# Kernel tuning notes

Measured on AMD Instinct MI355X. Metric: run time of the kernel, lower is better.

## Reference

```python
import jax, jax.numpy as jnp
import numpy as np
import math

EMBED_DIM = 2048
NUM_HEADS = 32
GROUPS = 4
HEAD_DIM = EMBED_DIM // NUM_HEADS  # 64
HPG = NUM_HEADS // GROUPS          # heads per group = 8


def setup_inputs() -> dict:
    key = jax.random.key(0)
    k_x, k_wq, k_bq, k_wkv, k_bkv = jax.random.split(key, 5)
    B, L = 4, 4096
    scale = 1.0 / math.sqrt(EMBED_DIM)
    return {
        "x": jax.random.normal(k_x, (B, L, EMBED_DIM), dtype=jnp.float32),
        "Wq": jax.random.normal(k_wq, (EMBED_DIM, EMBED_DIM), dtype=jnp.float32) * scale,
        "bq": jax.random.normal(k_bq, (EMBED_DIM,), dtype=jnp.float32) * 0.01,
        "Wkv": jax.random.normal(k_wkv, (EMBED_DIM, 2 * HEAD_DIM * GROUPS), dtype=jnp.float32) * scale,
        "bkv": jax.random.normal(k_bkv, (2 * HEAD_DIM * GROUPS,), dtype=jnp.float32) * 0.01,
    }


def reference(x, Wq, bq, Wkv, bkv):
    B, L, _ = x.shape
    # projections
    q = (x @ Wq + bq).reshape(B, L, GROUPS, HPG, HEAD_DIM)          # blghd
    kv = (x @ Wkv + bkv).reshape(B, L, GROUPS, 2, HEAD_DIM)
    k, v = kv[:, :, :, 0], kv[:, :, :, 1]                            # blgd
    # scores: q @ k^T with k of shape (..., 1, head_dim) -> (..., HPG, 1)
    scores = jnp.einsum("blghd,blgd->blgh", q, k)[..., None] / math.sqrt(HEAD_DIM)
    attn = jax.nn.softmax(scores, axis=-1)                           # size-1 axis -> ones
    # attn @ v: (..., HPG, 1) @ (..., 1, head_dim) -> (..., HPG, head_dim)
    out = attn * v[:, :, :, None, :]                                 # blghd
    return out.reshape(B, L, EMBED_DIM)
```

## Files before the change

kernel.cpp:

```cpp
#include <hip/hip_runtime.h>


#define EMBED 2048
#define NV 256
#define BM 32
#define BK 32
#define KITERS (EMBED / BK)
#define LDS_STRIDE 40
#define VS 260

typedef _Float16 half8 __attribute__((ext_vector_type(8)));
typedef _Float16 half4v __attribute__((ext_vector_type(4)));
typedef float f32x4 __attribute__((ext_vector_type(4)));

__global__ __launch_bounds__(256) void prep_b(const float* __restrict__ Wkv,
                                              _Float16* __restrict__ Bt) {
  __shared__ _Float16 T[256 * 72];
  const int t = threadIdx.x;
  const int kb = blockIdx.x * 64;
  const int vcol = ((t >> 6) * 128) + 64 + (t & 63);
  for (int i = 0; i < 64; ++i) {
    T[t * 72 + i] = (_Float16)Wkv[(size_t)(kb + i) * 512 + vcol];
  }
  __syncthreads();
  const half8* src = (const half8*)&T[t * 72];
  half8* dst = (half8*)&Bt[(size_t)t * EMBED + kb];
#pragma unroll
  for (int c = 0; c < 8; ++c) dst[c] = src[c];
}

__global__ __launch_bounds__(256, 2) void gqa_main(
    const float* __restrict__ x, const _Float16* __restrict__ Bt,
    const float* __restrict__ bkv, float* __restrict__ out) {
  extern __shared__ char smem[];
  _Float16* As = (_Float16*)smem;
  _Float16* Bs = (_Float16*)(smem + BM * LDS_STRIDE * 2);
  float* Vs = (float*)smem;

  const int tid = threadIdx.x;
  const int wave = tid >> 6;
  const int lane = tid & 63;
  const int lm = lane & 15;
  const int lq = lane >> 4;
  const int r0 = blockIdx.x * BM;

  const int am = tid >> 3, ak = (tid & 7) * 4;
  const float* ap = x + (size_t)(r0 + am) * EMBED + ak;
  const int bn = tid >> 2, bc = (tid & 3) * 8;
  const _Float16* bp = Bt + (size_t)bn * EMBED + bc;
  _Float16* awr = As + am * LDS_STRIDE + ak;
  _Float16* bwr = Bs + bn * LDS_STRIDE + bc;

  const _Float16* ard0 = As + (0 * 16 + lm) * LDS_STRIDE + lq * 8;
  const _Float16* ard1 = As + (1 * 16 + lm) * LDS_STRIDE + lq * 8;
  const _Float16* brd = Bs + (wave * 64 + lm) * LDS_STRIDE + lq * 8;

  f32x4 acc[2][4] = {};

  float4 aReg = *(const float4*)ap;
  half8 bReg0 = *(const half8*)(bp);
  half8 bReg1 = *(const half8*)(bp + 64 * EMBED);
  half8 bReg2 = *(const half8*)(bp + 128 * EMBED);
  half8 bReg3 = *(const half8*)(bp + 192 * EMBED);

  for (int kt = 0; kt < KITERS; ++kt) {
    half4v ah = {(_Float16)aReg.x, (_Float16)aReg.y, (_Float16)aReg.z,
                 (_Float16)aReg.w};
    *(half4v*)awr = ah;
    *(half8*)(bwr + 0 * 64 * LDS_STRIDE) = bReg0;
    *(half8*)(bwr + 1 * 64 * LDS_STRIDE) = bReg1;
    *(half8*)(bwr + 2 * 64 * LDS_STRIDE) = bReg2;
    *(half8*)(bwr + 3 * 64 * LDS_STRIDE) = bReg3;
    __syncthreads();

    if (kt + 1 < KITERS) {
      ap += BK;
      bp += BK;
      aReg = *(const float4*)ap;
      bReg0 = *(const half8*)(bp);
      bReg1 = *(const half8*)(bp + 64 * EMBED);
      bReg2 = *(const half8*)(bp + 128 * EMBED);
      bReg3 = *(const half8*)(bp + 192 * EMBED);
    }

    half8 a0 = *(const half8*)ard0;
    half8 a1 = *(const half8*)ard1;
#pragma unroll
    for (int ni = 0; ni < 4; ++ni) {
      half8 bf = *(const half8*)(brd + ni * 16 * LDS_STRIDE);
      acc[0][ni] = __builtin_amdgcn_mfma_f32_16x16x32_f16(a0, bf, acc[0][ni], 0, 0, 0);
      acc[1][ni] = __builtin_amdgcn_mfma_f32_16x16x32_f16(a1, bf, acc[1][ni], 0, 0, 0);
    }
    __syncthreads();
  }

#pragma unroll
  for (int ni = 0; ni < 4; ++ni) {
    const int ncol = wave * 64 + ni * 16 + lm;
    const float bias = bkv[((ncol >> 6) * 128) + 64 + (ncol & 63)];
#pragma unroll
    for (int mi = 0; mi < 2; ++mi) {
      f32x4 a = acc[mi][ni];
#pragma unroll
      for (int r = 0; r < 4; ++r) {
        Vs[(mi * 16 + lq * 4 + r) * VS + ncol] = a[r] + bias;
      }
    }
  }
  __syncthreads();

  float4* out4 = (float4*)out;
  const size_t obase = (size_t)r0 * 512;
#pragma unroll 4
  for (int i = 0; i < 64; ++i) {
    const int f = i * 256 + tid;
    const int m = f >> 9;
    const int c4 = f & 511;
    const int g = c4 >> 7;
    const int d4 = c4 & 15;
    float4 v = *(const float4*)&Vs[m * VS + g * 64 + d4 * 4];
    out4[obase + (size_t)f] = v;
  }
}

extern "C" void kernel_launch(void* const* d_in, const int* in_sizes, int n_in,
                              void* d_out, int out_size, void* d_ws, size_t ws_size,
                              hipStream_t stream) {
  const float* x = (const float*)d_in[0];
  const float* Wkv = (const float*)d_in[3];
  const float* bkv = (const float*)d_in[4];
  float* out = (float*)d_out;
  _Float16* Bt = (_Float16*)d_ws;

  prep_b<<<32, 256, 0, stream>>>(Wkv, Bt);

  const int mblocks = (4 * 4096) / BM;
  const size_t lds_bytes = 32 * VS * 4;
  gqa_main<<<mblocks, 256, lds_bytes, stream>>>(x, Bt, bkv, out);
}
```

Baseline: 301.5 us.

## Double-buffer B tiles in swizzled LDS and load A fragments directly from global

The GEMM main loop now uses BK=64 with two XOR-swizzled LDS buffers for the transposed weight tile. Weight loads are software-pipelined two iterations ahead, so there is one barrier per iteration instead of two. The x tile no longer goes through LDS: each lane reads its MFMA fragment straight from global memory as fp32 and converts it in registers. prep_b is also simplified to a direct per-thread load and pack over more blocks, and the LDS footprint grows to 64KB static, which may limit occupancy.

```diff
diff --git a/kernel.cpp b/kernel.cpp
--- a/kernel.cpp
+++ b/kernel.cpp
@@ -2,40 +2,40 @@
 
 
 #define EMBED 2048
-#define NV 256
 #define BM 32
-#define BK 32
+#define BK 64
 #define KITERS (EMBED / BK)
-#define LDS_STRIDE 40
+#define BUF_HALFS (256 * 64)
+
+typedef _Float16 half8 __attribute__((ext_vector_type(8)));
+typedef float f32x4 __attribute__((ext_vector_type(4)));
+
 #define VS 260
 
-typedef _Float16 half8 __attribute__((ext_vector_type(8)));
-typedef _Float16 half4v __attribute__((ext_vector_type(4)));
-typedef float f32x4 __attribute__((ext_vector_type(4)));
+__device__ __forceinline__ int bchunk(int row, int c) {
+  return row * 64 + ((c ^ (row & 7)) * 8);
+}
+
+#define ASM_BARRIER() asm volatile("s_waitcnt lgkmcnt(0)\ns_barrier" ::: "memory")
 
 __global__ __launch_bounds__(256) void prep_b(const float* __restrict__ Wkv,
                                               _Float16* __restrict__ Bt) {
-  __shared__ _Float16 T[256 * 72];
   const int t = threadIdx.x;
-  const int kb = blockIdx.x * 64;
+  const int kb = blockIdx.x * 8;
   const int vcol = ((t >> 6) * 128) + 64 + (t & 63);
-  for (int i = 0; i < 64; ++i) {
-    T[t * 72 + i] = (_Float16)Wkv[(size_t)(kb + i) * 512 + vcol];
-  }
-  __syncthreads();
-  const half8* src = (const half8*)&T[t * 72];
-  half8* dst = (half8*)&Bt[(size_t)t * EMBED + kb];
+  float v[8];
 #pragma unroll
-  for (int c = 0; c < 8; ++c) dst[c] = src[c];
+  for (int i = 0; i < 8; ++i) v[i] = Wkv[(size_t)(kb + i) * 512 + vcol];
+  half8 h;
+#pragma unroll
+  for (int i = 0; i < 8; ++i) h[i] = (_Float16)v[i];
+  *(half8*)&Bt[(size_t)t * EMBED + kb] = h;
 }
 
 __global__ __launch_bounds__(256, 2) void gqa_main(
     const float* __restrict__ x, const _Float16* __restrict__ Bt,
     const float* __restrict__ bkv, float* __restrict__ out) {
-  extern __shared__ char smem[];
-  _Float16* As = (_Float16*)smem;
-  _Float16* Bs = (_Float16*)(smem + BM * LDS_STRIDE * 2);
-  float* Vs = (float*)smem;
+  __shared__ _Float16 Bs[2 * BUF_HALFS];
 
   const int tid = threadIdx.x;
   const int wave = tid >> 6;
@@ -44,72 +44,93 @@
   const int lq = lane >> 4;
   const int r0 = blockIdx.x * BM;
 
-  const int am = tid >> 3, ak = (tid & 7) * 4;
-  const float* ap = x + (size_t)(r0 + am) * EMBED + ak;
-  const int bn = tid >> 2, bc = (tid & 3) * 8;
-  const _Float16* bp = Bt + (size_t)bn * EMBED + bc;
-  _Float16* awr = As + am * LDS_STRIDE + ak;
-  _Float16* bwr = Bs + bn * LDS_STRIDE + bc;
+  const int srow = tid >> 3;
+  const int sc = tid & 7;
+  const _Float16* bgp = Bt + (size_t)srow * EMBED + sc * 8;
+  int bso[8];
+#pragma unroll
+  for (int p = 0; p < 8; ++p) bso[p] = bchunk(srow + p * 32, sc);
 
-  const _Float16* ard0 = As + (0 * 16 + lm) * LDS_STRIDE + lq * 8;
-  const _Float16* ard1 = As + (1 * 16 + lm) * LDS_STRIDE + lq * 8;
-  const _Float16* brd = Bs + (wave * 64 + lm) * LDS_STRIDE + lq * 8;
+  const float* ag0 = x + (size_t)(r0 + lm) * EMBED + lq * 8;
 
+  half8 breg[2][8];
   f32x4 acc[2][4] = {};
 
-  float4 aReg = *(const float4*)ap;
-  half8 bReg0 = *(const half8*)(bp);
-  half8 bReg1 = *(const half8*)(bp + 64 * EMBED);
-  half8 bReg2 = *(const half8*)(bp + 128 * EMBED);
-  half8 bReg3 = *(const half8*)(bp + 192 * EMBED);
+#define LOADB(kt, R)                                                       \
+  {                                                                        \
+    const _Float16* p_ = bgp + (kt) * BK;                                  \
+    _Pragma("unroll") for (int i_ = 0; i_ < 8; ++i_)                       \
+        R[i_] = *(const half8*)(p_ + (size_t)i_ * 32 * EMBED);             \
+  }
+#define STOREB(R, buf)                                                     \
+  {                                                                        \
+    _Float16* b_ = Bs + (buf)*BUF_HALFS;                                   \
+    _Pragma("unroll") for (int i_ = 0; i_ < 8; ++i_)                       \
+        *(half8*)(b_ + bso[i_]) = R[i_];                                   \
+  }
+
+  LOADB(0, breg[0]);
+  STOREB(breg[0], 0);
+  LOADB(1, breg[1]);
+  ASM_BARRIER();
 
   for (int kt = 0; kt < KITERS; ++kt) {
-    half4v ah = {(_Float16)aReg.x, (_Float16)aReg.y, (_Float16)aReg.z,
-                 (_Float16)aReg.w};
-    *(half4v*)awr = ah;
-    *(half8*)(bwr + 0 * 64 * LDS_STRIDE) = bReg0;
-    *(half8*)(bwr + 1 * 64 * LDS_STRIDE) = bReg1;
-    *(half8*)(bwr + 2 * 64 * LDS_STRIDE) = bReg2;
-    *(half8*)(bwr + 3 * 64 * LDS_STRIDE) = bReg3;
-    __syncthreads();
+    const int cur = kt & 1;
 
-    if (kt + 1 < KITERS) {
-      ap += BK;
-      bp += BK;
-      aReg = *(const float4*)ap;
-      bReg0 = *(const half8*)(bp);
-      bReg1 = *(const half8*)(bp + 64 * EMBED);
-      bReg2 = *(const half8*)(bp + 128 * EMBED);
-      bReg3 = *(const half8*)(bp + 192 * EMBED);
+    f32x4 a[2][2][2];
+#pragma unroll
+    for (int mi = 0; mi < 2; ++mi)
+#pragma unroll
+      for (int ks = 0; ks < 2; ++ks) {
+        const float* p = ag0 + (size_t)mi * 16 * EMBED + kt * BK + ks * 32;
+        a[mi][ks][0] = *(const f32x4*)p;
+        a[mi][ks][1] = *(const f32x4*)(p + 4);
+      }
+
+    if (kt + 1 < KITERS) STOREB(breg[(kt + 1) & 1], 1 - cur);
+    if (kt + 2 < KITERS) LOADB(kt + 2, breg[kt & 1]);
+
+    const _Float16* bb = Bs + cur * BUF_HALFS;
+#pragma unroll
+    for (int ks = 0; ks < 2; ++ks) {
+      half8 af[2];
+#pragma unroll
+      for (int mi = 0; mi < 2; ++mi)
+#pragma unroll
+        for (int j = 0; j < 4; ++j) {
+          af[mi][j] = (_Float16)a[mi][ks][0][j];
+          af[mi][4 + j] = (_Float16)a[mi][ks][1][j];
+        }
+#pragma unroll
+      for (int ni = 0; ni < 4; ++ni) {
+        const int row = wave * 64 + ni * 16 + lm;
+        half8 bf = *(const half8*)(bb + bchunk(row, ks * 4 + lq));
+        acc[0][ni] =
+            __builtin_amdgcn_mfma_f32_16x16x32_f16(af[0], bf, acc[0][ni], 0, 0, 0);
+        acc[1][ni] =
+            __builtin_amdgcn_mfma_f32_16x16x32_f16(af[1], bf, acc[1][ni], 0, 0, 0);
+      }
     }
-
-    half8 a0 = *(const half8*)ard0;
-    half8 a1 = *(const half8*)ard1;
-#pragma unroll
-    for (int ni = 0; ni < 4; ++ni) {
-      half8 bf = *(const half8*)(brd + ni * 16 * LDS_STRIDE);
-      acc[0][ni] = __builtin_amdgcn_mfma_f32_16x16x32_f16(a0, bf, acc[0][ni], 0, 0, 0);
-      acc[1][ni] = __builtin_amdgcn_mfma_f32_16x16x32_f16(a1, bf, acc[1][ni], 0, 0, 0);
-    }
-    __syncthreads();
+    ASM_BARRIER();
   }
 
+  float* Vs = (float*)Bs;
 #pragma unroll
   for (int ni = 0; ni < 4; ++ni) {
     const int ncol = wave * 64 + ni * 16 + lm;
     const float bias = bkv[((ncol >> 6) * 128) + 64 + (ncol & 63)];
 #pragma unroll
     for (int mi = 0; mi < 2; ++mi) {
-      f32x4 a = acc[mi][ni];
+      f32x4 v = acc[mi][ni];
 #pragma unroll
       for (int r = 0; r < 4; ++r) {
-        Vs[(mi * 16 + lq * 4 + r) * VS + ncol] = a[r] + bias;
+        Vs[(mi * 16 + lq * 4 + r) * VS + ncol] = v[r] + bias;
       }
     }
   }
   __syncthreads();
 
-  float4* out4 = (float4*)out;
+  f32x4* out4 = (f32x4*)out;
   const size_t obase = (size_t)r0 * 512;
 #pragma unroll 4
   for (int i = 0; i < 64; ++i) {
@@ -118,8 +139,7 @@
     const int c4 = f & 511;
     const int g = c4 >> 7;
     const int d4 = c4 & 15;
-    float4 v = *(const float4*)&Vs[m * VS + g * 64 + d4 * 4];
-    out4[obase + (size_t)f] = v;
+    out4[obase + (size_t)f] = *(const f32x4*)&Vs[m * VS + g * 64 + d4 * 4];
   }
 }
 
@@ -132,9 +152,6 @@
   float* out = (float*)d_out;
   _Float16* Bt = (_Float16*)d_ws;
 
-  prep_b<<<32, 256, 0, stream>>>(Wkv, Bt);
-
-  const int mblocks = (4 * 4096) / BM;
-  const size_t lds_bytes = 32 * VS * 4;
-  gqa_main<<<mblocks, 256, lds_bytes, stream>>>(x, Bt, bkv, out);
+  prep_b<<<256, 256, 0, stream>>>(Wkv, Bt);
+  gqa_main<<<(4 * 4096) / BM, 256, 0, stream>>>(x, Bt, bkv, out);
 }
```

Result: slower. 441.5 us (+46.5%).
